# Kernel optimization log

Measured on AMD Instinct MI355X. Metric: run time of the kernel, lower is better.

The kernel has to match this reference:

```python
import jax, jax.numpy as jnp
import numpy as np

N_NODES = 100000
N_EDGES = 1600000
IN_DIM = 128
N_HID = 128


def setup_inputs() -> dict:
    key = jax.random.key(0)
    k1, k2, k3, k4 = jax.random.split(key, 4)
    node_feature = jax.random.normal(k1, (N_NODES, IN_DIM), dtype=jnp.float32)
    edge_index = jax.random.randint(k2, (2, N_EDGES), 0, N_NODES, dtype=jnp.int64)
    # GCN layer weights (glorot-ish scale)
    W1 = jax.random.normal(k3, (IN_DIM, N_HID), dtype=jnp.float32) / np.sqrt(IN_DIM)
    b1 = jnp.zeros((N_HID,), dtype=jnp.float32)
    W2 = jax.random.normal(k4, (N_HID, N_HID), dtype=jnp.float32) / np.sqrt(N_HID)
    b2 = jnp.zeros((N_HID,), dtype=jnp.float32)
    return {"node_feature": node_feature, "edge_index": edge_index,
            "W1": W1, "b1": b1, "W2": W2, "b2": b2}


def _gcn_layer(x, W, b, row, col, n_nodes):
    """GCNConv: x' = D^-1/2 (A + I) D^-1/2 (x W) + b, symmetric norm with self-loops."""
    xt = x @ W  # [N, out]
    ones = jnp.ones(row.shape[0], dtype=xt.dtype)
    deg = jnp.zeros((n_nodes,), dtype=xt.dtype).at[col].add(ones) + 1.0  # +1 self-loop
    dinv = jax.lax.rsqrt(deg)  # [N]
    norm = dinv[row] * dinv[col]  # [E]
    # gather messages from source (row), scatter-add into destination (col)
    agg = jnp.zeros_like(xt).at[col].add(xt[row] * norm[:, None])
    agg = agg + xt * (dinv * dinv)[:, None]  # self-loop contribution
    return agg + b


def reference(node_feature, edge_index, W1, b1, W2, b2):
    row, col = edge_index[0], edge_index[1]
    n = node_feature.shape[0]
    h = _gcn_layer(node_feature, W1, b1, row, col, n)
    # F.dropout with training=False is identity (eval-mode reference)
    h = _gcn_layer(h, W2, b2, row, col, n)
    return h
```

## Files before the change

### kernel.cpp

```cpp
#include <hip/hip_runtime.h>

typedef unsigned short ushort_t;
typedef __attribute__((ext_vector_type(8))) short short8;
typedef __attribute__((ext_vector_type(8))) unsigned short us8v;
typedef __attribute__((ext_vector_type(4))) float f32x4;

__device__ __forceinline__ float b2f(unsigned short u) {
    union { unsigned int i; float f; } v; v.i = ((unsigned int)u) << 16; return v.f;
}
__device__ __forceinline__ unsigned short f2b(float f) {
    union { float f; unsigned int i; } v; v.f = f;
    unsigned int r = (v.i + 0x7FFF + ((v.i >> 16) & 1)) >> 16;
    return (unsigned short)r;
}

__device__ __forceinline__ void load_edge(const int* __restrict__ ei, int e, int E,
                                          int is64, int& s, int& d) {
    if (is64) { s = ei[2 * e]; d = ei[2 * (E + e)]; }
    else      { s = ei[e];     d = ei[E + e]; }
}

__global__ void k_hist(const int* __restrict__ ei, int E, unsigned N,
                       int* __restrict__ bhist, int BSH, int NB) {
    __shared__ int lh[256];
    int t = threadIdx.x;
    for (int b = t; b < NB; b += 256) lh[b] = 0;
    int z = 0;
    for (int i = t; i < 512; i += 256) z |= ei[2 * i + 1];
    int is64 = (__syncthreads_or(z) == 0);
    int e0 = blockIdx.x * 4096;
    #pragma unroll
    for (int i = 0; i < 16; ++i) {
        int e = e0 + i * 256 + t;
        if (e < E) {
            int s, d; load_edge(ei, e, E, is64, s, d);
            if ((unsigned)s < N && (unsigned)d < N) atomicAdd(&lh[d >> BSH], 1);
        }
    }
    __syncthreads();
    for (int b = t; b < NB; b += 256) { int v = lh[b]; if (v) atomicAdd(&bhist[b], v); }
}

__global__ void k_scanb(const int* __restrict__ bhist, int NB,
                        int* __restrict__ bkbase, int* __restrict__ bkcur) {
    __shared__ int sd[256];
    int t = threadIdx.x;
    int v0 = (t < NB) ? bhist[t] : 0;
    sd[t] = v0;
    for (int o = 1; o < 256; o <<= 1) {
        __syncthreads();
        int v = (t >= o) ? sd[t - o] : 0;
        __syncthreads();
        sd[t] += v;
    }
    __syncthreads();
    if (t < NB) { int ex = sd[t] - v0; bkbase[t] = ex; bkcur[t] = ex; }
}

__global__ __launch_bounds__(256) void k_bucket(const int* __restrict__ ei, int E, unsigned N,
                                                int* __restrict__ bkcur,
                                                int* __restrict__ bs, int* __restrict__ bd,
                                                int BSH, int NB) {
    __shared__ int lss[4096];
    __shared__ int ldd[4096];
    __shared__ int lhist[256];
    __shared__ int lcur[256];
    int t = threadIdx.x;
    int e0 = blockIdx.x * 4096;
    for (int b = t; b < NB; b += 256) lhist[b] = 0;
    int z = 0;
    for (int i = t; i < 512; i += 256) z |= ei[2 * i + 1];
    int is64 = (__syncthreads_or(z) == 0);
    #pragma unroll
    for (int i = 0; i < 16; ++i) {
        int idx = i * 256 + t, e = e0 + idx;
        int s = -1, d = -1;
        if (e < E) {
            load_edge(ei, e, E, is64, s, d);
            if (!((unsigned)s < N && (unsigned)d < N)) d = -1;
        }
        lss[idx] = s; ldd[idx] = d;
        if (d >= 0) atomicAdd(&lhist[d >> BSH], 1);
    }
    __syncthreads();
    for (int b = t; b < NB; b += 256) {
        int v = lhist[b];
        lcur[b] = v ? atomicAdd(&bkcur[b], v) : 0;
    }
    __syncthreads();
    #pragma unroll
    for (int i = 0; i < 16; ++i) {
        int idx = i * 256 + t;
        int d = ldd[idx];
        if (d >= 0) {
            int p = atomicAdd(&lcur[d >> BSH], 1);
            bs[p] = lss[idx]; bd[p] = d;
        }
    }
}

__global__ void k_count2(const int* __restrict__ bd, const int* __restrict__ bkbase,
                         const int* __restrict__ bkcur, int N, int BSH,
                         int* __restrict__ cnt) {
    __shared__ int lc[512];
    int b = blockIdx.x, t = threadIdx.x;
    int nbase = b << BSH;
    int nn = min(1 << BSH, N - nbase);
    for (int j = t; j < nn; j += 256) lc[j] = 0;
    __syncthreads();
    int s0 = bkbase[b], s1 = bkcur[b];
    for (int i = s0 + t; i < s1; i += 256) atomicAdd(&lc[bd[i] - nbase], 1);
    __syncthreads();
    for (int j = t; j < nn; j += 256) cnt[nbase + j] = lc[j];
}

__global__ void k_assign(int* __restrict__ cnt, int N,
                         int* __restrict__ pos, float* __restrict__ dinv,
                         int* __restrict__ cursor, int* __restrict__ srcs,
                         int padidx) {
    __shared__ int sd[256];
    __shared__ int sbase;
    int t = threadIdx.x;
    int n = blockIdx.x * 256 + t;
    int c = (n < N) ? cnt[n] : 0;
    int cp = (c + 7) & ~7;
    sd[t] = cp;
    for (int o = 1; o < 256; o <<= 1) {
        __syncthreads();
        int v = (t >= o) ? sd[t - o] : 0;
        __syncthreads();
        sd[t] += v;
    }
    __syncthreads();
    if (t == 255) sbase = atomicAdd(cursor, sd[255]);
    __syncthreads();
    if (n < N) {
        int st = sbase + sd[t] - cp;
        pos[n] = st;
        dinv[n] = rsqrtf((float)c + 1.0f);
        cnt[n] = cp;
        for (int q = c; q < cp; ++q) srcs[st + q] = padidx;
    }
}

__global__ void k_fill2(const int* __restrict__ bs, const int* __restrict__ bd,
                        const int* __restrict__ bkbase, const int* __restrict__ bkcur,
                        const int* __restrict__ pos, int N, int BSH,
                        int* __restrict__ srcs) {
    __shared__ int lcur[512];
    int b = blockIdx.x, t = threadIdx.x;
    int nbase = b << BSH;
    int nn = min(1 << BSH, N - nbase);
    for (int j = t; j < nn; j += 256) lcur[j] = pos[nbase + j];
    __syncthreads();
    int s0 = bkbase[b], s1 = bkcur[b];
    for (int i = s0 + t; i < s1; i += 256) {
        int d = bd[i];
        int p = atomicAdd(&lcur[d - nbase], 1);
        srcs[p] = bs[i];
    }
}

__global__ void k_transpose(const float* __restrict__ W1, const float* __restrict__ W2,
                            ushort_t* __restrict__ WT, ushort_t* __restrict__ xt,
                            int N) {
    if (blockIdx.x == 2) {
        int t = threadIdx.x;
        if (t < 128) xt[((size_t)N << 7) + t] = 0;
        return;
    }
    const float* src = blockIdx.x ? W2 : W1;
    ushort_t* dst = WT + blockIdx.x * 16384;
    for (int i = threadIdx.x; i < 16384; i += 256) {
        int n = i >> 7, k = i & 127;
        dst[i] = f2b(src[k * 128 + n]);
    }
}

__global__ __launch_bounds__(256) void k_gemm(const float* __restrict__ A,
                                              const ushort_t* __restrict__ WT,
                                              ushort_t* __restrict__ C,
                                              const float* __restrict__ dinv, int M) {
    __shared__ __align__(16) ushort_t sA[64 * 136];
    __shared__ __align__(16) ushort_t sW[128 * 136];
    int t = threadIdx.x;
    int row0 = blockIdx.x * 64;

    #pragma unroll
    for (int it = 0; it < 8; ++it) {
        int flat = (it * 256 + t) * 8;
        int n = flat >> 7, k = flat & 127;
        uint4 v = *(const uint4*)(WT + flat);
        *(uint4*)(&sW[n * 136 + k]) = v;
    }
    #pragma unroll
    for (int it = 0; it < 4; ++it) {
        int flat = (it * 256 + t) * 8;
        int r = flat >> 7, cc = flat & 127;
        int row = row0 + r; if (row > M - 1) row = M - 1;
        const float* p = A + (size_t)row * 128 + cc;
        float4 f0 = *(const float4*)p;
        float4 f1 = *(const float4*)(p + 4);
        ushort_t tmp[8] __attribute__((aligned(16)));
        tmp[0] = f2b(f0.x); tmp[1] = f2b(f0.y); tmp[2] = f2b(f0.z); tmp[3] = f2b(f0.w);
        tmp[4] = f2b(f1.x); tmp[5] = f2b(f1.y); tmp[6] = f2b(f1.z); tmp[7] = f2b(f1.w);
        *(uint4*)(&sA[r * 136 + cc]) = *(const uint4*)tmp;
    }
    __syncthreads();

    int w = t >> 6, lane = t & 63;
    int m = lane & 15, quad = lane >> 4;

    f32x4 acc[8] = {};
    #pragma unroll
    for (int k0 = 0; k0 < 128; k0 += 32) {
        short8 af = *(const short8*)(&sA[(w * 16 + m) * 136 + k0 + quad * 8]);
        #pragma unroll
        for (int tt = 0; tt < 8; ++tt) {
            short8 bf = *(const short8*)(&sW[(tt * 16 + m) * 136 + k0 + quad * 8]);
            acc[tt] = __builtin_amdgcn_mfma_f32_16x16x32_bf16(af, bf, acc[tt], 0, 0, 0);
        }
    }
    #pragma unroll
    for (int r = 0; r < 4; ++r) {
        int row = row0 + w * 16 + quad * 4 + r;
        if (row < M) {
            float dd = dinv[row];
            #pragma unroll
            for (int tt = 0; tt < 8; ++tt)
                C[(size_t)row * 128 + tt * 16 + m] = f2b(dd * acc[tt][r]);
        }
    }
}

__global__ __launch_bounds__(256) void k_agg(const ushort_t* __restrict__ xt,
                                             const float* __restrict__ bias,
                                             float* __restrict__ out,
                                             const int* __restrict__ pos,
                                             const int* __restrict__ cnts,
                                             const float* __restrict__ dinv,
                                             const int* __restrict__ srcs, int N) {
    int lane = threadIdx.x & 63;
    int slot = lane >> 4, j = lane & 15;
    int d = (blockIdx.x << 2) + (threadIdx.x >> 6);
    if (d >= N) return;
    int cn = cnts[d];
    int start = pos[d];
    float dd = dinv[d];
    us8v vs = *(const us8v*)(xt + ((size_t)d << 7) + (j << 3));
    float4 bb0 = *(const float4*)(bias + (j << 3));
    float4 bb1 = *(const float4*)(bias + (j << 3) + 4);

    float a0 = 0.f, a1 = 0.f, a2 = 0.f, a3 = 0.f;
    float a4 = 0.f, a5 = 0.f, a6 = 0.f, a7 = 0.f;

    for (int base = 0; base < cn; base += 64) {
        int n = cn - base; if (n > 64) n = 64;
        int sv = 0;
        if (lane < n) sv = srcs[start + base + lane];
        #pragma unroll 2
        for (int c = 0; c < n; c += 8) {
            int s0 = __shfl(sv, c + slot);
            int s1 = __shfl(sv, c + 4 + slot);
            us8v v0 = *(const us8v*)(xt + ((size_t)s0 << 7) + (j << 3));
            us8v v1 = *(const us8v*)(xt + ((size_t)s1 << 7) + (j << 3));
            a0 += b2f(v0[0]); a1 += b2f(v0[1]); a2 += b2f(v0[2]); a3 += b2f(v0[3]);
            a4 += b2f(v0[4]); a5 += b2f(v0[5]); a6 += b2f(v0[6]); a7 += b2f(v0[7]);
            a0 += b2f(v1[0]); a1 += b2f(v1[1]); a2 += b2f(v1[2]); a3 += b2f(v1[3]);
            a4 += b2f(v1[4]); a5 += b2f(v1[5]); a6 += b2f(v1[6]); a7 += b2f(v1[7]);
        }
    }
    a0 += __shfl_xor(a0, 32); a1 += __shfl_xor(a1, 32);
    a2 += __shfl_xor(a2, 32); a3 += __shfl_xor(a3, 32);
    a4 += __shfl_xor(a4, 32); a5 += __shfl_xor(a5, 32);
    a6 += __shfl_xor(a6, 32); a7 += __shfl_xor(a7, 32);
    a0 += __shfl_xor(a0, 16); a1 += __shfl_xor(a1, 16);
    a2 += __shfl_xor(a2, 16); a3 += __shfl_xor(a3, 16);
    a4 += __shfl_xor(a4, 16); a5 += __shfl_xor(a5, 16);
    a6 += __shfl_xor(a6, 16); a7 += __shfl_xor(a7, 16);

    if (slot == 0) {
        float4 o0, o1;
        o0.x = dd * (a0 + b2f(vs[0])) + bb0.x;
        o0.y = dd * (a1 + b2f(vs[1])) + bb0.y;
        o0.z = dd * (a2 + b2f(vs[2])) + bb0.z;
        o0.w = dd * (a3 + b2f(vs[3])) + bb0.w;
        o1.x = dd * (a4 + b2f(vs[4])) + bb1.x;
        o1.y = dd * (a5 + b2f(vs[5])) + bb1.y;
        o1.z = dd * (a6 + b2f(vs[6])) + bb1.z;
        o1.w = dd * (a7 + b2f(vs[7])) + bb1.w;
        float4* po = (float4*)(out + ((size_t)d << 7) + (j << 3));
        po[0] = o0; po[1] = o1;
    }
}


extern "C" void kernel_launch(void* const* d_in, const int* in_sizes, int n_in,
                              void* d_out, int out_size, void* d_ws, size_t ws_size,
                              hipStream_t stream) {
    const float* x  = (const float*)d_in[0];
    const int*   ei = (const int*)d_in[1];
    const float* W1 = (const float*)d_in[2];
    const float* b1 = (const float*)d_in[3];
    const float* W2 = (const float*)d_in[4];
    const float* b2 = (const float*)d_in[5];
    float* out = (float*)d_out;

    const int N = in_sizes[0] / 128;
    const int E = in_sizes[1] / 2;

    int BSH = 9;
    int NB = (N + (1 << BSH) - 1) >> BSH;
    while (NB > 256) { BSH++; NB = (N + (1 << BSH) - 1) >> BSH; }

    char* ws = (char*)d_ws;
    size_t o = 0;
    auto take = [&](size_t bytes) { size_t r = o; o = (o + bytes + 255) & ~(size_t)255; return r; };
    size_t o_bhist  = take(256 * 4);
    size_t o_cursor = take(4);
    size_t zero_end = o;
    size_t o_bkbase = take(256 * 4);
    size_t o_bkcur  = take(256 * 4);
    size_t o_cnt    = take((size_t)N * 4);
    size_t o_pos    = take((size_t)N * 4);
    size_t o_dinv   = take((size_t)N * 4);
    size_t o_srcs   = take(((size_t)E + 7 * (size_t)N + 64) * 4);
    size_t o_WT     = take(2 * 128 * 128 * 2);
    size_t big_sz   = (size_t)E * 8 > (size_t)(N + 1) * 256 ? (size_t)E * 8
                                                            : (size_t)(N + 1) * 256;
    size_t o_big    = take(big_sz);
    (void)ws_size;

    int*      bhist  = (int*)(ws + o_bhist);
    int*      cursor = (int*)(ws + o_cursor);
    int*      bkbase = (int*)(ws + o_bkbase);
    int*      bkcur  = (int*)(ws + o_bkcur);
    int*      cnt    = (int*)(ws + o_cnt);
    int*      pos    = (int*)(ws + o_pos);
    float*    dinv   = (float*)(ws + o_dinv);
    int*      srcs   = (int*)(ws + o_srcs);
    ushort_t* WT     = (ushort_t*)(ws + o_WT);
    int*      bs     = (int*)(ws + o_big);
    int*      bd     = (int*)(ws + o_big) + E;
    ushort_t* xt     = (ushort_t*)(ws + o_big);
    float*    h      = out;

    hipMemsetAsync(d_ws, 0, zero_end, stream);

    int gE = (E + 4095) / 4096;
    int gN = (N + 255) / 256;
    k_hist<<<gE, 256, 0, stream>>>(ei, E, (unsigned)N, bhist, BSH, NB);
    k_scanb<<<1, 256, 0, stream>>>(bhist, NB, bkbase, bkcur);
    k_bucket<<<gE, 256, 0, stream>>>(ei, E, (unsigned)N, bkcur, bs, bd, BSH, NB);
    k_count2<<<NB, 256, 0, stream>>>(bd, bkbase, bkcur, N, BSH, cnt);
    k_assign<<<gN, 256, 0, stream>>>(cnt, N, pos, dinv, cursor, srcs, N);
    k_fill2<<<NB, 256, 0, stream>>>(bs, bd, bkbase, bkcur, pos, N, BSH, srcs);
    k_transpose<<<3, 256, 0, stream>>>(W1, W2, WT, xt, N);

    int gG = (N + 63) / 64;
    int gA = (N + 3) / 4;
    k_gemm<<<gG, 256, 0, stream>>>(x, WT, xt, dinv, N);
    k_agg<<<gA, 256, 0, stream>>>(xt, b1, h, pos, cnt, dinv, srcs, N);
    k_gemm<<<gG, 256, 0, stream>>>(h, WT + 16384, xt, dinv, N);
    k_agg<<<gA, 256, 0, stream>>>(xt, b2, out, pos, cnt, dinv, srcs, N);
}
```

Before: 352.5 us.

## Store intermediate hidden layer in bf16 and software-pipeline aggregation gathers

The first aggregation now writes its hidden output as bf16 instead of fp32. The second GEMM reads that bf16 directly, which removes the fp32 write and read plus the conversion in the GEMM load. The aggregation loop is restructured so the next pair of neighbour rows is loaded before the current pair is accumulated, to overlap gather latency. The edge loader reads int64 indices as 64-bit words, and the edge-size detection is factored into a helper. The first-layer output was already rounded to bf16 inside the GEMM, so accuracy changes little.

```diff
diff --git a/kernel.cpp b/kernel.cpp
--- a/kernel.cpp
+++ b/kernel.cpp
@@ -16,8 +16,18 @@
 
 __device__ __forceinline__ void load_edge(const int* __restrict__ ei, int e, int E,
                                           int is64, int& s, int& d) {
-    if (is64) { s = ei[2 * e]; d = ei[2 * (E + e)]; }
-    else      { s = ei[e];     d = ei[E + e]; }
+    if (is64) {
+        const long long* el = (const long long*)ei;
+        s = (int)el[e]; d = (int)el[E + e];
+    } else {
+        s = ei[e]; d = ei[E + e];
+    }
+}
+
+__device__ __forceinline__ int detect64(const int* __restrict__ ei, int t) {
+    int z = 0;
+    for (int i = t; i < 512; i += 256) z |= ei[2 * i + 1];
+    return (__syncthreads_or(z) == 0);
 }
 
 __global__ void k_hist(const int* __restrict__ ei, int E, unsigned N,
@@ -25,9 +35,7 @@
     __shared__ int lh[256];
     int t = threadIdx.x;
     for (int b = t; b < NB; b += 256) lh[b] = 0;
-    int z = 0;
-    for (int i = t; i < 512; i += 256) z |= ei[2 * i + 1];
-    int is64 = (__syncthreads_or(z) == 0);
+    int is64 = detect64(ei, t);
     int e0 = blockIdx.x * 4096;
     #pragma unroll
     for (int i = 0; i < 16; ++i) {
@@ -68,9 +76,7 @@
     int t = threadIdx.x;
     int e0 = blockIdx.x * 4096;
     for (int b = t; b < NB; b += 256) lhist[b] = 0;
-    int z = 0;
-    for (int i = t; i < 512; i += 256) z |= ei[2 * i + 1];
-    int is64 = (__syncthreads_or(z) == 0);
+    int is64 = detect64(ei, t);
     #pragma unroll
     for (int i = 0; i < 16; ++i) {
         int idx = i * 256 + t, e = e0 + idx;
@@ -177,7 +183,8 @@
     }
 }
 
-__global__ __launch_bounds__(256) void k_gemm(const float* __restrict__ A,
+template <bool ABF>
+__global__ __launch_bounds__(256) void k_gemm(const void* __restrict__ Ap,
                                               const ushort_t* __restrict__ WT,
                                               ushort_t* __restrict__ C,
                                               const float* __restrict__ dinv, int M) {
@@ -198,13 +205,20 @@
         int flat = (it * 256 + t) * 8;
         int r = flat >> 7, cc = flat & 127;
         int row = row0 + r; if (row > M - 1) row = M - 1;
-        const float* p = A + (size_t)row * 128 + cc;
-        float4 f0 = *(const float4*)p;
-        float4 f1 = *(const float4*)(p + 4);
-        ushort_t tmp[8] __attribute__((aligned(16)));
-        tmp[0] = f2b(f0.x); tmp[1] = f2b(f0.y); tmp[2] = f2b(f0.z); tmp[3] = f2b(f0.w);
-        tmp[4] = f2b(f1.x); tmp[5] = f2b(f1.y); tmp[6] = f2b(f1.z); tmp[7] = f2b(f1.w);
-        *(uint4*)(&sA[r * 136 + cc]) = *(const uint4*)tmp;
+        if (ABF) {
+            const ushort_t* A = (const ushort_t*)Ap;
+            us8v v = *(const us8v*)(A + ((size_t)row << 7) + cc);
+            *(us8v*)(&sA[r * 136 + cc]) = v;
+        } else {
+            const float* A = (const float*)Ap;
+            const float* p = A + (size_t)row * 128 + cc;
+            float4 f0 = *(const float4*)p;
+            float4 f1 = *(const float4*)(p + 4);
+            ushort_t tmp[8] __attribute__((aligned(16)));
+            tmp[0] = f2b(f0.x); tmp[1] = f2b(f0.y); tmp[2] = f2b(f0.z); tmp[3] = f2b(f0.w);
+            tmp[4] = f2b(f1.x); tmp[5] = f2b(f1.y); tmp[6] = f2b(f1.z); tmp[7] = f2b(f1.w);
+            *(uint4*)(&sA[r * 136 + cc]) = *(const uint4*)tmp;
+        }
     }
     __syncthreads();
 
@@ -233,9 +247,10 @@
     }
 }
 
+template <bool OBF>
 __global__ __launch_bounds__(256) void k_agg(const ushort_t* __restrict__ xt,
                                              const float* __restrict__ bias,
-                                             float* __restrict__ out,
+                                             void* __restrict__ outp,
                                              const int* __restrict__ pos,
                                              const int* __restrict__ cnts,
                                              const float* __restrict__ dinv,
@@ -258,17 +273,25 @@
         int n = cn - base; if (n > 64) n = 64;
         int sv = 0;
         if (lane < n) sv = srcs[start + base + lane];
-        #pragma unroll 2
-        for (int c = 0; c < n; c += 8) {
-            int s0 = __shfl(sv, c + slot);
-            int s1 = __shfl(sv, c + 4 + slot);
-            us8v v0 = *(const us8v*)(xt + ((size_t)s0 << 7) + (j << 3));
-            us8v v1 = *(const us8v*)(xt + ((size_t)s1 << 7) + (j << 3));
+        int s0 = __shfl(sv, slot);
+        int s1 = __shfl(sv, 4 + slot);
+        us8v v0 = *(const us8v*)(xt + ((size_t)s0 << 7) + (j << 3));
+        us8v v1 = *(const us8v*)(xt + ((size_t)s1 << 7) + (j << 3));
+        for (int c = 8; c < n; c += 8) {
+            int t0 = __shfl(sv, c + slot);
+            int t1 = __shfl(sv, c + 4 + slot);
+            us8v w0 = *(const us8v*)(xt + ((size_t)t0 << 7) + (j << 3));
+            us8v w1 = *(const us8v*)(xt + ((size_t)t1 << 7) + (j << 3));
             a0 += b2f(v0[0]); a1 += b2f(v0[1]); a2 += b2f(v0[2]); a3 += b2f(v0[3]);
             a4 += b2f(v0[4]); a5 += b2f(v0[5]); a6 += b2f(v0[6]); a7 += b2f(v0[7]);
             a0 += b2f(v1[0]); a1 += b2f(v1[1]); a2 += b2f(v1[2]); a3 += b2f(v1[3]);
             a4 += b2f(v1[4]); a5 += b2f(v1[5]); a6 += b2f(v1[6]); a7 += b2f(v1[7]);
-        }
+            v0 = w0; v1 = w1;
+        }
+        a0 += b2f(v0[0]); a1 += b2f(v0[1]); a2 += b2f(v0[2]); a3 += b2f(v0[3]);
+        a4 += b2f(v0[4]); a5 += b2f(v0[5]); a6 += b2f(v0[6]); a7 += b2f(v0[7]);
+        a0 += b2f(v1[0]); a1 += b2f(v1[1]); a2 += b2f(v1[2]); a3 += b2f(v1[3]);
+        a4 += b2f(v1[4]); a5 += b2f(v1[5]); a6 += b2f(v1[6]); a7 += b2f(v1[7]);
     }
     a0 += __shfl_xor(a0, 32); a1 += __shfl_xor(a1, 32);
     a2 += __shfl_xor(a2, 32); a3 += __shfl_xor(a3, 32);
@@ -280,17 +303,25 @@
     a6 += __shfl_xor(a6, 16); a7 += __shfl_xor(a7, 16);
 
     if (slot == 0) {
-        float4 o0, o1;
-        o0.x = dd * (a0 + b2f(vs[0])) + bb0.x;
-        o0.y = dd * (a1 + b2f(vs[1])) + bb0.y;
-        o0.z = dd * (a2 + b2f(vs[2])) + bb0.z;
-        o0.w = dd * (a3 + b2f(vs[3])) + bb0.w;
-        o1.x = dd * (a4 + b2f(vs[4])) + bb1.x;
-        o1.y = dd * (a5 + b2f(vs[5])) + bb1.y;
-        o1.z = dd * (a6 + b2f(vs[6])) + bb1.z;
-        o1.w = dd * (a7 + b2f(vs[7])) + bb1.w;
-        float4* po = (float4*)(out + ((size_t)d << 7) + (j << 3));
-        po[0] = o0; po[1] = o1;
+        float o0 = dd * (a0 + b2f(vs[0])) + bb0.x;
+        float o1 = dd * (a1 + b2f(vs[1])) + bb0.y;
+        float o2 = dd * (a2 + b2f(vs[2])) + bb0.z;
+        float o3 = dd * (a3 + b2f(vs[3])) + bb0.w;
+        float o4 = dd * (a4 + b2f(vs[4])) + bb1.x;
+        float o5 = dd * (a5 + b2f(vs[5])) + bb1.y;
+        float o6 = dd * (a6 + b2f(vs[6])) + bb1.z;
+        float o7 = dd * (a7 + b2f(vs[7])) + bb1.w;
+        if (OBF) {
+            ushort_t tmp[8] __attribute__((aligned(16)));
+            tmp[0] = f2b(o0); tmp[1] = f2b(o1); tmp[2] = f2b(o2); tmp[3] = f2b(o3);
+            tmp[4] = f2b(o4); tmp[5] = f2b(o5); tmp[6] = f2b(o6); tmp[7] = f2b(o7);
+            *(us8v*)((ushort_t*)outp + ((size_t)d << 7) + (j << 3)) = *(const us8v*)tmp;
+        } else {
+            float4 q0 = { o0, o1, o2, o3 };
+            float4 q1 = { o4, o5, o6, o7 };
+            float4* po = (float4*)((float*)outp + ((size_t)d << 7) + (j << 3));
+            po[0] = q0; po[1] = q1;
+        }
     }
 }
 
@@ -343,12 +374,15 @@
     int*      bs     = (int*)(ws + o_big);
     int*      bd     = (int*)(ws + o_big) + E;
     ushort_t* xt     = (ushort_t*)(ws + o_big);
-    float*    h      = out;
+    ushort_t* hbf    = (ushort_t*)d_out;
 
     hipMemsetAsync(d_ws, 0, zero_end, stream);
 
     int gE = (E + 4095) / 4096;
     int gN = (N + 255) / 256;
+    int gG = (N + 63) / 64;
+    int gA = (N + 3) / 4;
+
     k_hist<<<gE, 256, 0, stream>>>(ei, E, (unsigned)N, bhist, BSH, NB);
     k_scanb<<<1, 256, 0, stream>>>(bhist, NB, bkbase, bkcur);
     k_bucket<<<gE, 256, 0, stream>>>(ei, E, (unsigned)N, bkcur, bs, bd, BSH, NB);
@@ -357,10 +391,8 @@
     k_fill2<<<NB, 256, 0, stream>>>(bs, bd, bkbase, bkcur, pos, N, BSH, srcs);
     k_transpose<<<3, 256, 0, stream>>>(W1, W2, WT, xt, N);
 
-    int gG = (N + 63) / 64;
-    int gA = (N + 3) / 4;
-    k_gemm<<<gG, 256, 0, stream>>>(x, WT, xt, dinv, N);
-    k_agg<<<gA, 256, 0, stream>>>(xt, b1, h, pos, cnt, dinv, srcs, N);
-    k_gemm<<<gG, 256, 0, stream>>>(h, WT + 16384, xt, dinv, N);
-    k_agg<<<gA, 256, 0, stream>>>(xt, b2, out, pos, cnt, dinv, srcs, N);
-}
+    k_gemm<false><<<gG, 256, 0, stream>>>(x, WT, xt, dinv, N);
+    k_agg<true><<<gA, 256, 0, stream>>>(xt, b1, hbf, pos, cnt, dinv, srcs, N);
+    k_gemm<true><<<gG, 256, 0, stream>>>(hbf, WT + 16384, xt, dinv, N);
+    k_agg<false><<<gA, 256, 0, stream>>>(xt, b2, out, pos, cnt, dinv, srcs, N);
+}
```

After: 345.6 us. No clear change (-1.9%).
